# Kernel tuning notes

Measured on AMD Instinct MI355X. Metric: run time of the kernel, lower is better.

Reference implementation:

```python
import jax, jax.numpy as jnp
import numpy as np

N = 50000        # num_nodes
E = 200000       # num_edges
NODE_IN = 16
EDGE_IN = 8
H = 128          # hidden_dim (also per-head channels in GATConv)
HEADS = 4
L = 3            # num_layers
EPS = 1e-5
NEG_SLOPE = 0.2  # PyG GATConv default


def layer_norm(x, g, b):
    mu = jnp.mean(x, axis=-1, keepdims=True)
    v = jnp.var(x, axis=-1, keepdims=True)
    return (x - mu) * jax.lax.rsqrt(v + EPS) * g + b


def batch_norm_eval(x, g, b, rm, rv):
    return (x - rm) * jax.lax.rsqrt(rv + EPS) * g + b


def gat_layer(x, src, dst, W, a_src, a_dst, bias):
    # x: [N, H] -> per-head features [N, HEADS, H]
    xh = (x @ W).reshape(N, HEADS, H)
    al_src = jnp.sum(xh * a_src, axis=-1)  # [N, HEADS]
    al_dst = jnp.sum(xh * a_dst, axis=-1)  # [N, HEADS]
    alpha = jax.nn.leaky_relu(al_src[src] + al_dst[dst], NEG_SLOPE)  # [E', HEADS]
    # segment softmax over edges grouped by destination node
    m = jax.ops.segment_max(alpha, dst, num_segments=N)
    e = jnp.exp(alpha - m[dst])
    s = jax.ops.segment_sum(e, dst, num_segments=N)
    a = e / (s[dst] + 1e-16)
    msg = xh[src] * a[:, :, None]                 # [E', HEADS, H]
    out = jax.ops.segment_sum(msg, dst, num_segments=N)  # [N, HEADS, H]
    return jnp.mean(out, axis=1) + bias           # concat=False -> head mean


def setup_inputs() -> dict:
    key = jax.random.key(0)
    ks = jax.random.split(key, 24)
    s = 0.1
    inp = {
        "x": jax.random.normal(ks[0], (N, NODE_IN), jnp.float32),
        "edge_index": jax.random.randint(ks[1], (2, E), 0, N, jnp.int32),
        "edge_attr": jax.random.normal(ks[2], (E, EDGE_IN), jnp.float32),
        "shock_mask_nodes": jax.random.randint(ks[3], (N,), 0, 2, jnp.int32),
        # node encoder
        "enc_w": jax.random.normal(ks[4], (NODE_IN + 2, H), jnp.float32) * s,
        "enc_b": jnp.zeros((H,), jnp.float32),
        "enc_ln_g": jnp.ones((H,), jnp.float32),
        "enc_ln_b": jnp.zeros((H,), jnp.float32),
        # GAT layers (stacked over L)
        "gat_w": jax.random.normal(ks[5], (L, H, HEADS * H), jnp.float32) * s,
        "gat_att_src": jax.random.normal(ks[6], (L, HEADS, H), jnp.float32) * s,
        "gat_att_dst": jax.random.normal(ks[7], (L, HEADS, H), jnp.float32) * s,
        "gat_bias": jnp.zeros((L, H), jnp.float32),
        # BatchNorm (eval mode: running stats)
        "bn_g": jnp.ones((L, H), jnp.float32),
        "bn_b": jnp.zeros((L, H), jnp.float32),
        "bn_mean": jax.random.normal(ks[8], (L, H), jnp.float32) * 0.01,
        "bn_var": jnp.ones((L, H), jnp.float32),
        # edge MLP: (2H + EDGE_IN) -> H -> H//2 -> 1
        "em1_w": jax.random.normal(ks[9], (2 * H + EDGE_IN, H), jnp.float32) * s,
        "em1_b": jnp.zeros((H,), jnp.float32),
        "em_ln_g": jnp.ones((H,), jnp.float32),
        "em_ln_b": jnp.zeros((H,), jnp.float32),
        "em2_w": jax.random.normal(ks[10], (H, H // 2), jnp.float32) * s,
        "em2_b": jnp.zeros((H // 2,), jnp.float32),
        "em3_w": jax.random.normal(ks[11], (H // 2, 1), jnp.float32) * s,
        "em3_b": jnp.zeros((1,), jnp.float32),
    }
    return inp


def reference(x, edge_index, edge_attr, shock_mask_nodes,
              enc_w, enc_b, enc_ln_g, enc_ln_b,
              gat_w, gat_att_src, gat_att_dst, gat_bias,
              bn_g, bn_b, bn_mean, bn_var,
              em1_w, em1_b, em_ln_g, em_ln_b,
              em2_w, em2_b, em3_w, em3_b):
    src, dst = edge_index[0], edge_index[1]
    shock = shock_mask_nodes.astype(jnp.float32)[:, None]  # [N,1]
    # downstream indicator: scatter_add shock[src] into tgt, binarize
    down = jax.ops.segment_sum(shock[src, 0], dst, num_segments=N)
    down = (down > 0).astype(jnp.float32)[:, None]
    xa = jnp.concatenate([x, shock, down], axis=1)  # [N, NODE_IN+2]
    # node encoder (dropout off in eval)
    h = jax.nn.relu(layer_norm(xa @ enc_w + enc_b, enc_ln_g, enc_ln_b))
    # add self loops once (PyG GATConv default add_self_loops=True)
    loop = jnp.arange(N, dtype=src.dtype)
    src_sl = jnp.concatenate([src, loop])
    dst_sl = jnp.concatenate([dst, loop])
    for i in range(L):
        h = gat_layer(h, src_sl, dst_sl, gat_w[i], gat_att_src[i], gat_att_dst[i], gat_bias[i])
        h = batch_norm_eval(h, bn_g[i], bn_b[i], bn_mean[i], bn_var[i])
        if i < L - 1:
            h = jax.nn.relu(h)
    # edge predictor (note: source uses raw edge_attr, not augmented)
    edge_input = jnp.concatenate([h[src], h[dst], edge_attr], axis=1)  # [E, 2H+EDGE_IN]
    z = jax.nn.relu(layer_norm(edge_input @ em1_w + em1_b, em_ln_g, em_ln_b))
    z = jax.nn.relu(z @ em2_w + em2_b)
    delta = (z @ em3_w + em3_b)[:, 0]  # [E]
    return delta
```

## Files before the change

kernel.cpp:

```cpp
#include <hip/hip_runtime.h>
#include <hip/hip_bf16.h>


#define N_NODES 50000
#define N_EDGES 200000
#define ETOT    (N_EDGES + N_NODES)
#define HID     128
#define LN_EPS  1e-5f
#define NEG     0.2f
#define NSB     196

typedef __hip_bfloat16 bf16;
typedef __attribute__((ext_vector_type(8))) short v8s;
typedef __attribute__((ext_vector_type(4))) float v4f;
#define MFMA(a, b, c) __builtin_amdgcn_mfma_f32_16x16x32_bf16(a, b, c, 0, 0, 0)

__device__ __forceinline__ float b2f(unsigned short s) {
    return __uint_as_float(((unsigned int)s) << 16);
}
__device__ __forceinline__ unsigned short f2b(float f) {
    __hip_bfloat16 h = __float2bfloat16(f);
    return *reinterpret_cast<unsigned short*>(&h);
}
__device__ __forceinline__ unsigned int pack2(float a, float b) {
    return (unsigned int)f2b(a) | ((unsigned int)f2b(b) << 16);
}
__device__ __forceinline__ float pread(const void* p, size_t i, int isbf) {
    if (isbf) return b2f(((const unsigned short*)p)[i]);
    return ((const float*)p)[i];
}

__global__ void k_fill(float* out, int n, float v) {
    int i = blockIdx.x * blockDim.x + threadIdx.x;
    if (i < n) out[i] = v;
}

__global__ void k_detect(const unsigned short* __restrict__ xbuf,
                         int* __restrict__ flag) {
    int sane = 0;
    for (int j = threadIdx.x; j < 4096; j += 64) {
        unsigned short v = xbuf[2 * j];
        int e = (v >> 7) & 0xFF;
        if (v == 0 || (e > 96 && e < 160)) sane++;
    }
    for (int off = 32; off > 0; off >>= 1) sane += __shfl_down(sane, off);
    if (threadIdx.x == 0) flag[0] = (sane * 10 >= 4096 * 9) ? 1 : 0;
}

struct PrepArgs {
    const void *encw, *encb, *enlg, *enlb, *gatw, *asrc, *adst, *bias,
               *bng, *bnb, *bnm, *bnv, *em1w, *em1b, *emlg, *emlb,
               *em2w, *em2b, *em3w, *em3b;
};
#define PREP_ITEMS (150000 + 8193 + 1024 + 196608 + 32768 + 8192 + 3072)
__global__ void k_prep(PrepArgs a, float* __restrict__ pool,
                       unsigned short* __restrict__ gwt,
                       unsigned short* __restrict__ uvt,
                       unsigned short* __restrict__ w2t,
                       float* __restrict__ wl,
                       float* __restrict__ down, int* __restrict__ deg,
                       int* __restrict__ fill, const int* __restrict__ flag) {
    int i = blockIdx.x * 256 + threadIdx.x;
    int bf = flag[0];
    if (i < 150000) {
        int which = i / 50000, idx = i - which * 50000;
        if (which == 0) down[idx] = 0.f;
        else if (which == 1) deg[idx] = 0;
        else fill[idx] = 0;
        return;
    }
    i -= 150000;
    if (i < 8193) {
        const void* s; int off;
        if      (i < 2304) { s = a.encw; off = 0;    }
        else if (i < 2432) { s = a.encb; off = 2304; }
        else if (i < 2560) { s = a.enlg; off = 2432; }
        else if (i < 2688) { s = a.enlb; off = 2560; }
        else if (i < 4224) { s = a.asrc; off = 2688; }
        else if (i < 5760) { s = a.adst; off = 4224; }
        else if (i < 6144) { s = a.bias; off = 5760; }
        else if (i < 6528) { s = a.bng;  off = 6144; }
        else if (i < 6912) { s = a.bnb;  off = 6528; }
        else if (i < 7296) { s = a.bnm;  off = 6912; }
        else if (i < 7680) { s = a.bnv;  off = 7296; }
        else if (i < 7808) { s = a.em1b; off = 7680; }
        else if (i < 7936) { s = a.emlg; off = 7808; }
        else if (i < 8064) { s = a.emlb; off = 7936; }
        else if (i < 8128) { s = a.em2b; off = 8064; }
        else if (i < 8192) { s = a.em3w; off = 8128; }
        else               { s = a.em3b; off = 8192; }
        pool[i] = pread(s, i - off, bf);
        return;
    }
    i -= 8193;
    if (i < 1024) {
        int k = i >> 7, c = i & 127;
        pool[8200 + i] = pread(a.em1w, (size_t)(256 + k) * 128 + c, bf);
        return;
    }
    i -= 1024;
    if (i < 196608) {
        int L = i >> 16, rem = i & 65535, c = rem >> 9, k = rem & 511;
        gwt[i] = f2b(pread(a.gatw,
            (size_t)L * 65536 + (size_t)(k & 127) * 512 + (k >> 7) * 128 + c, bf));
        return;
    }
    i -= 196608;
    if (i < 32768) {
        int n = i >> 7, k = i & 127;
        float v = (n < 128) ? pread(a.em1w, (size_t)k * 128 + n, bf)
                            : pread(a.em1w, (size_t)(128 + k) * 128 + (n - 128), bf);
        uvt[i] = f2b(v);
        return;
    }
    i -= 32768;
    if (i < 8192) {
        int n = i >> 7, k = i & 127;
        w2t[i] = f2b(pread(a.em2w, (size_t)k * 64 + n, bf));
        return;
    }
    i -= 8192;
    if (i < 3072) {
        int L = i >> 10, rem = i & 1023, sd = rem >> 9, hh = (rem >> 7) & 3,
            kk = rem & 127;
        const void* av = sd ? a.adst : a.asrc;
        float acc = 0.f;
        for (int c = 0; c < 128; c++)
            acc += pread(a.gatw,
                       (size_t)L * 65536 + (size_t)kk * 512 + hh * 128 + c, bf)
                 * pread(av, (size_t)L * 512 + hh * 128 + c, bf);
        wl[i] = acc;
    }
}

__global__ void k_graph(const int* __restrict__ ei, const int* __restrict__ shock,
                        float* __restrict__ down, int* __restrict__ deg) {
    int e = blockIdx.x * blockDim.x + threadIdx.x;
    if (e < ETOT) {
        int d = (e < N_EDGES) ? ei[N_EDGES + e] : (e - N_EDGES);
        atomicAdd(&deg[d], 1);
        if (e < N_EDGES && shock[ei[e]] != 0) down[d] = 1.f;
    }
}

__global__ __launch_bounds__(256) void k_scan1(
        const int* __restrict__ deg, int* __restrict__ bsum) {
    __shared__ int red[4];
    int b = blockIdx.x, t = threadIdx.x, lane = t & 63, w = t >> 6;
    int idx = b * 256 + t;
    int v = (idx < N_NODES) ? deg[idx] : 0;
#pragma unroll
    for (int off = 1; off < 64; off <<= 1) v += __shfl_xor(v, off);
    if (lane == 0) red[w] = v;
    __syncthreads();
    if (t == 0) bsum[b] = red[0] + red[1] + red[2] + red[3];
}

__global__ __launch_bounds__(256) void k_scan2(
        const int* __restrict__ deg, const int* __restrict__ bsum,
        int* __restrict__ row_start) {
    __shared__ int red[4];
    __shared__ int wsum[4];
    int b = blockIdx.x, t = threadIdx.x, lane = t & 63, w = t >> 6;
    int pv = (t < b) ? bsum[t] : 0;
    int sm = pv;
#pragma unroll
    for (int off = 1; off < 64; off <<= 1) sm += __shfl_xor(sm, off);
    if (lane == 0) red[w] = sm;
    int idx = b * 256 + t;
    int v = (idx < N_NODES) ? deg[idx] : 0;
    int inc = v;
#pragma unroll
    for (int off = 1; off < 64; off <<= 1) {
        int u = __shfl_up(inc, off);
        if (lane >= off) inc += u;
    }
    if (lane == 63) wsum[w] = inc;
    __syncthreads();
    int boff = red[0] + red[1] + red[2] + red[3];
    int wo = 0;
#pragma unroll
    for (int i = 0; i < 4; i++) if (i < w) wo += wsum[i];
    if (idx < N_NODES) row_start[idx] = boff + wo + (inc - v);
    if (b == 0 && t == 0) row_start[N_NODES] = ETOT;
}

__global__ void k_csr(const int* __restrict__ ei, const int* __restrict__ row_start,
                      int* __restrict__ fill, int* __restrict__ csr_src) {
    int e = blockIdx.x * blockDim.x + threadIdx.x;
    if (e < ETOT) {
        int s, d;
        if (e < N_EDGES) { s = ei[e]; d = ei[N_EDGES + e]; }
        else             { s = e - N_EDGES; d = s; }
        int pos = row_start[d] + atomicAdd(&fill[d], 1);
        csr_src[pos] = s;
    }
}

__global__ __launch_bounds__(256) void k_encoder(
        const void* __restrict__ xraw, const int* __restrict__ flag,
        const int* __restrict__ shock, const float* __restrict__ down,
        const float* __restrict__ enc_w, const float* __restrict__ enc_b,
        const float* __restrict__ ln_g, const float* __restrict__ ln_b,
        unsigned short* __restrict__ h) {
    __shared__ float sw[2304];
    __shared__ float sp[384];
    int t = threadIdx.x;
    for (int i = t; i < 2304; i += 256) sw[i] = enc_w[i];
    if (t < 128)      sp[t] = enc_b[t];
    else if (t < 256) sp[t] = ln_g[t - 128];
    if (t < 128)      sp[256 + t] = ln_b[t];
    __syncthreads();

    int w = t >> 6, l = t & 63;
    int n = blockIdx.x * 4 + w;
    int bf = flag[0];
    int c0 = 2 * l, c1 = c0 + 1;

    float xv = (l < 16) ? pread(xraw, (size_t)n * 16 + l, bf) : 0.f;
    float xs = (float)shock[n];
    float xd = down[n];

    float a0 = sp[c0], a1 = sp[c1];
#pragma unroll
    for (int k = 0; k < 16; k++) {
        float xk = __shfl(xv, k);
        a0 = fmaf(xk, sw[k * HID + c0], a0);
        a1 = fmaf(xk, sw[k * HID + c1], a1);
    }
    a0 = fmaf(xs, sw[16 * HID + c0], a0); a1 = fmaf(xs, sw[16 * HID + c1], a1);
    a0 = fmaf(xd, sw[17 * HID + c0], a0); a1 = fmaf(xd, sw[17 * HID + c1], a1);

    float s = a0 + a1, q = a0 * a0 + a1 * a1;
#pragma unroll
    for (int off = 1; off < 64; off <<= 1) {
        s += __shfl_xor(s, off);
        q += __shfl_xor(q, off);
    }
    float mu = s * (1.f / 128.f);
    float var = q * (1.f / 128.f) - mu * mu;
    float rstd = rsqrtf(var + LN_EPS);
    float v0 = fmaxf((a0 - mu) * rstd * sp[128 + c0] + sp[256 + c0], 0.f);
    float v1 = fmaxf((a1 - mu) * rstd * sp[128 + c1] + sp[256 + c1], 0.f);
    *(unsigned int*)&h[(size_t)n * HID + c0] = pack2(v0, v1);
}

__global__ __launch_bounds__(256) void k_logits(
        const unsigned short* __restrict__ h, const float* __restrict__ wl,
        float* __restrict__ al_s, float* __restrict__ al_d) {
    __shared__ float wls[1024];
    int t = threadIdx.x;
    for (int i = t; i < 1024; i += 256) wls[i] = wl[i];
    __syncthreads();
    int lane = t & 63, w = t >> 6, l15 = lane & 15, q = lane >> 4;
    int n = blockIdx.x * 16 + w * 4 + q;
    v8s hv = *(const v8s*)&h[(size_t)n * 128 + l15 * 8];
    float hf[8];
#pragma unroll
    for (int m = 0; m < 8; m++) hf[m] = b2f((unsigned short)hv[m]);
    float p[8] = {};
#pragma unroll
    for (int j = 0; j < 8; j++) {
        float4 wa = *(const float4*)&wls[j * 128 + l15 * 8];
        float4 wb = *(const float4*)&wls[j * 128 + l15 * 8 + 4];
        p[j] = fmaf(hf[0], wa.x, p[j]); p[j] = fmaf(hf[1], wa.y, p[j]);
        p[j] = fmaf(hf[2], wa.z, p[j]); p[j] = fmaf(hf[3], wa.w, p[j]);
        p[j] = fmaf(hf[4], wb.x, p[j]); p[j] = fmaf(hf[5], wb.y, p[j]);
        p[j] = fmaf(hf[6], wb.z, p[j]); p[j] = fmaf(hf[7], wb.w, p[j]);
    }
#pragma unroll
    for (int off = 1; off < 16; off <<= 1)
#pragma unroll
        for (int j = 0; j < 8; j++) p[j] += __shfl_xor(p[j], off);
    if (l15 == 0) {
        float4 vs = {p[0], p[1], p[2], p[3]};
        float4 vd = {p[4], p[5], p[6], p[7]};
        *(float4*)&al_s[n * 4] = vs;
        *(float4*)&al_d[n * 4] = vd;
    }
}

__global__ __launch_bounds__(256) void k_agg2(
        const unsigned short* __restrict__ h, const float* __restrict__ al_src,
        const float* __restrict__ al_dst,
        const int* __restrict__ row_start, const int* __restrict__ csr_src,
        unsigned short* __restrict__ agg) {
    int w = threadIdx.x >> 6, l = threadIdx.x & 63;
    int n = blockIdx.x * 4 + w;
    int r0 = row_start[n], r1 = row_start[n + 1];
    float4 ad4 = *(const float4*)&al_dst[n * 4];
    float s0 = 0.f, s1 = 0.f, s2 = 0.f, s3 = 0.f;
    float acc[4][2] = {};
    int last = r1 - 1;
    int i0 = csr_src[r0];
    int i1 = csr_src[(r0 + 1 < r1) ? r0 + 1 : last];
    float4 aC = *(const float4*)&al_src[i0 * 4];
    unsigned int hC = *(const unsigned int*)&h[(size_t)i0 * 128 + 2 * l];
    for (int j = r0; j < r1; j++) {
        int i2 = csr_src[(j + 2 < r1) ? j + 2 : last];
        float4 aN = *(const float4*)&al_src[i1 * 4];
        unsigned int hN = *(const unsigned int*)&h[(size_t)i1 * 128 + 2 * l];
        float h0 = b2f((unsigned short)(hC & 0xFFFFu));
        float h1 = b2f((unsigned short)(hC >> 16));
        float t0 = aC.x + ad4.x; t0 = (t0 >= 0.f) ? t0 : NEG * t0;
        float t1 = aC.y + ad4.y; t1 = (t1 >= 0.f) ? t1 : NEG * t1;
        float t2 = aC.z + ad4.z; t2 = (t2 >= 0.f) ? t2 : NEG * t2;
        float t3 = aC.w + ad4.w; t3 = (t3 >= 0.f) ? t3 : NEG * t3;
        float e0 = __expf(t0), e1 = __expf(t1), e2 = __expf(t2), e3 = __expf(t3);
        s0 += e0; s1 += e1; s2 += e2; s3 += e3;
        acc[0][0] = fmaf(e0, h0, acc[0][0]); acc[0][1] = fmaf(e0, h1, acc[0][1]);
        acc[1][0] = fmaf(e1, h0, acc[1][0]); acc[1][1] = fmaf(e1, h1, acc[1][1]);
        acc[2][0] = fmaf(e2, h0, acc[2][0]); acc[2][1] = fmaf(e2, h1, acc[2][1]);
        acc[3][0] = fmaf(e3, h0, acc[3][0]); acc[3][1] = fmaf(e3, h1, acc[3][1]);
        aC = aN; hC = hN; i1 = i2;
    }
    float inv0 = 1.f / (s0 + 1e-16f), inv1 = 1.f / (s1 + 1e-16f);
    float inv2 = 1.f / (s2 + 1e-16f), inv3 = 1.f / (s3 + 1e-16f);
    size_t base = (size_t)n * 512 + 2 * l;
    *(unsigned int*)&agg[base]       = pack2(acc[0][0] * inv0, acc[0][1] * inv0);
    *(unsigned int*)&agg[base + 128] = pack2(acc[1][0] * inv1, acc[1][1] * inv1);
    *(unsigned int*)&agg[base + 256] = pack2(acc[2][0] * inv2, acc[2][1] * inv2);
    *(unsigned int*)&agg[base + 384] = pack2(acc[3][0] * inv3, acc[3][1] * inv3);
}

__global__ __launch_bounds__(256, 4) void k_gemm2(
        const unsigned short* __restrict__ A,
        const unsigned short* __restrict__ Wt,
        const float* __restrict__ bias,
        const float* __restrict__ bn_g, const float* __restrict__ bn_b,
        const float* __restrict__ bn_m, const float* __restrict__ bn_v,
        unsigned short* __restrict__ hout, int relu_flag) {
    __shared__ __align__(16) unsigned short As[64 * 136];
    int t = threadIdx.x;
    int lane = t & 63, w = t >> 6, l15 = lane & 15, q = lane >> 4;
    int m0 = blockIdx.x * 64;
    int c0 = w * 32 + 2 * l15, c1 = c0 + 1;

    v4f acc[4][2] = {};
#pragma unroll 1
    for (int kc = 0; kc < 4; kc++) {
        if (kc) __syncthreads();
#pragma unroll
        for (int it = 0; it < 4; it++) {
            int c = t + it * 256;
            int row = c >> 4, ch = c & 15;
            v8s val = {0, 0, 0, 0, 0, 0, 0, 0};
            if (m0 + row < N_NODES)
                val = *(const v8s*)&A[(size_t)(m0 + row) * 512 + kc * 128 + ch * 8];
            *(v8s*)&As[row * 136 + ch * 8] = val;
        }
        __syncthreads();
#pragma unroll
        for (int kt = 0; kt < 4; kt++) {
            v8s b0 = *(const v8s*)&Wt[(size_t)c0 * 512 + kc * 128 + kt * 32 + q * 8];
            v8s b1 = *(const v8s*)&Wt[(size_t)c1 * 512 + kc * 128 + kt * 32 + q * 8];
#pragma unroll
            for (int mt = 0; mt < 4; mt++) {
                v8s a = *(const v8s*)&As[(mt * 16 + l15) * 136 + kt * 32 + q * 8];
                acc[mt][0] = MFMA(a, b0, acc[mt][0]);
                acc[mt][1] = MFMA(a, b1, acc[mt][1]);
            }
        }
    }
    float bi0 = bias[c0], bi1 = bias[c1];
    float sc0 = rsqrtf(bn_v[c0] + LN_EPS) * bn_g[c0];
    float sc1 = rsqrtf(bn_v[c1] + LN_EPS) * bn_g[c1];
    float sh0 = bn_b[c0] - bn_m[c0] * sc0;
    float sh1 = bn_b[c1] - bn_m[c1] * sc1;
#pragma unroll
    for (int mt = 0; mt < 4; mt++)
#pragma unroll
        for (int r = 0; r < 4; r++) {
            int node = m0 + mt * 16 + q * 4 + r;
            if (node < N_NODES) {
                float v0 = (0.25f * acc[mt][0][r] + bi0) * sc0 + sh0;
                float v1 = (0.25f * acc[mt][1][r] + bi1) * sc1 + sh1;
                if (relu_flag) { v0 = fmaxf(v0, 0.f); v1 = fmaxf(v1, 0.f); }
                *(unsigned int*)&hout[(size_t)node * 128 + c0] = pack2(v0, v1);
            }
        }
}

__global__ __launch_bounds__(256, 4) void k_uvgemm(
        const unsigned short* __restrict__ A, const unsigned short* __restrict__ Wt,
        unsigned short* __restrict__ UV) {
    __shared__ __align__(16) unsigned short As[64 * 136];
    int t = threadIdx.x;
    int lane = t & 63, w = t >> 6, l15 = lane & 15, q = lane >> 4;
    int m0 = blockIdx.x * 64, n0 = blockIdx.y * 128;
    int c0 = n0 + w * 32 + 2 * l15;

    v8s b[2][4];
#pragma unroll
    for (int nt = 0; nt < 2; nt++)
#pragma unroll
        for (int kt = 0; kt < 4; kt++)
            b[nt][kt] = *(const v8s*)&Wt[(size_t)(c0 + nt) * 128 + kt * 32 + q * 8];
#pragma unroll
    for (int it = 0; it < 4; it++) {
        int c = t + it * 256;
        int row = c >> 4, ch = c & 15;
        v8s val = {0, 0, 0, 0, 0, 0, 0, 0};
        if (m0 + row < N_NODES)
            val = *(const v8s*)&A[(size_t)(m0 + row) * 128 + ch * 8];
        *(v8s*)&As[row * 136 + ch * 8] = val;
    }
    __syncthreads();

    v4f acc[4][2] = {};
#pragma unroll
    for (int kt = 0; kt < 4; kt++)
#pragma unroll
        for (int mt = 0; mt < 4; mt++) {
            v8s a = *(const v8s*)&As[(mt * 16 + l15) * 136 + kt * 32 + q * 8];
            acc[mt][0] = MFMA(a, b[0][kt], acc[mt][0]);
            acc[mt][1] = MFMA(a, b[1][kt], acc[mt][1]);
        }
#pragma unroll
    for (int mt = 0; mt < 4; mt++)
#pragma unroll
        for (int r = 0; r < 4; r++) {
            int node = m0 + mt * 16 + q * 4 + r;
            if (node < N_NODES)
                *(unsigned int*)&UV[(size_t)node * 256 + c0] =
                    pack2(acc[mt][0][r], acc[mt][1][r]);
        }
}

__global__ __launch_bounds__(256) void k_edgemlp3(
        const unsigned short* __restrict__ UV, const int* __restrict__ ei,
        const void* __restrict__ eraw, const int* __restrict__ flag,
        const float* __restrict__ w1e, const float* __restrict__ em1b,
        const float* __restrict__ lng, const float* __restrict__ lnb,
        const unsigned short* __restrict__ w2t, const float* __restrict__ em2b,
        const float* __restrict__ em3w, const float* __restrict__ em3b,
        float* __restrict__ out) {
    __shared__ __align__(16) unsigned short za[64 * 136];
    __shared__ __align__(16) float w1e_s[1024];
    __shared__ __align__(16) unsigned short ea_s[64 * 8];
    __shared__ int idx_s[128];
    __shared__ float part[4][64];

    int t = threadIdx.x;
    int lane = t & 63, w = t >> 6, l15 = lane & 15, q = lane >> 4;
    int e0 = blockIdx.x * 64;
    int bf = flag[0];
    int cb = l15 * 8;

    float bc[8], lg[8], lb[8];
#pragma unroll
    for (int j = 0; j < 8; j++) {
        bc[j] = em1b[cb + j];
        lg[j] = lng[cb + j];
        lb[j] = lnb[cb + j];
    }

    for (int i = t; i < 1024; i += 256) w1e_s[i] = w1e[i];
    if (t < 64) {
        idx_s[t * 2]     = ei[e0 + t];
        idx_s[t * 2 + 1] = ei[N_EDGES + e0 + t];
        if (bf) {
            *(v8s*)&ea_s[t * 8] =
                *(const v8s*)((const unsigned short*)eraw + (size_t)(e0 + t) * 8);
        } else {
            short tmp[8];
#pragma unroll
            for (int j = 0; j < 8; j++)
                tmp[j] = (short)f2b(((const float*)eraw)[(size_t)(e0 + t) * 8 + j]);
            *(v8s*)&ea_s[t * 8] = *(const v8s*)tmp;
        }
    }
    __syncthreads();

    int elC = w * 16 + q;
    {
        int srcC = idx_s[elC * 2], dstC = idx_s[elC * 2 + 1];
        v8s uuC = *(const v8s*)&UV[(size_t)srcC * 256 + cb];
        v8s vvC = *(const v8s*)&UV[(size_t)dstC * 256 + 128 + cb];
        v8s eaC = *(const v8s*)&ea_s[elC * 8];
#pragma unroll 1
        for (int i = 0; i < 4; i++) {
            v8s uuN = uuC, vvN = vvC, eaN = eaC;
            if (i < 3) {
                int elN = elC + 4;
                int srcN = idx_s[elN * 2], dstN = idx_s[elN * 2 + 1];
                uuN = *(const v8s*)&UV[(size_t)srcN * 256 + cb];
                vvN = *(const v8s*)&UV[(size_t)dstN * 256 + 128 + cb];
                eaN = *(const v8s*)&ea_s[elN * 8];
            }
            float eaf[8];
#pragma unroll
            for (int k = 0; k < 8; k++) eaf[k] = b2f((unsigned short)eaC[k]);
            float e[8] = {};
#pragma unroll
            for (int k = 0; k < 8; k++) {
                float4 wa = *(const float4*)&w1e_s[k * 128 + cb];
                float4 wb = *(const float4*)&w1e_s[k * 128 + cb + 4];
                e[0] = fmaf(eaf[k], wa.x, e[0]);
                e[1] = fmaf(eaf[k], wa.y, e[1]);
                e[2] = fmaf(eaf[k], wa.z, e[2]);
                e[3] = fmaf(eaf[k], wa.w, e[3]);
                e[4] = fmaf(eaf[k], wb.x, e[4]);
                e[5] = fmaf(eaf[k], wb.y, e[5]);
                e[6] = fmaf(eaf[k], wb.z, e[6]);
                e[7] = fmaf(eaf[k], wb.w, e[7]);
            }
            float z[8];
            float s = 0.f, qq = 0.f;
#pragma unroll
            for (int j = 0; j < 8; j++) {
                float zz = b2f((unsigned short)uuC[j]) + b2f((unsigned short)vvC[j])
                         + e[j] + bc[j];
                z[j] = zz;
                s += zz;
                qq = fmaf(zz, zz, qq);
            }
#pragma unroll
            for (int off = 1; off < 16; off <<= 1) {
                s  += __shfl_xor(s, off);
                qq += __shfl_xor(qq, off);
            }
            float mu = s * (1.f / 128.f);
            float var = qq * (1.f / 128.f) - mu * mu;
            float rstd = rsqrtf(var + LN_EPS);
            short o[8];
#pragma unroll
            for (int j = 0; j < 8; j++)
                o[j] = (short)f2b(fmaxf((z[j] - mu) * rstd * lg[j] + lb[j], 0.f));
            *(v8s*)&za[elC * 136 + cb] = *(const v8s*)o;
            elC += 4; uuC = uuN; vvC = vvN; eaC = eaN;
        }
    }
    __syncthreads();

    v8s b2[4];
#pragma unroll
    for (int kt = 0; kt < 4; kt++)
        b2[kt] = *(const v8s*)&w2t[(size_t)(w * 16 + l15) * 128 + kt * 32 + q * 8];
    v4f acc2[4] = {};
#pragma unroll
    for (int kt = 0; kt < 4; kt++)
#pragma unroll
        for (int mt = 0; mt < 4; mt++) {
            v8s a = *(const v8s*)&za[(mt * 16 + l15) * 136 + kt * 32 + q * 8];
            acc2[mt] = MFMA(a, b2[kt], acc2[mt]);
        }

    {
        int col = w * 16 + l15;
        float b2c = em2b[col], w3c = em3w[col];
#pragma unroll
        for (int mt = 0; mt < 4; mt++)
#pragma unroll
            for (int r = 0; r < 4; r++) {
                float vv = fmaxf(acc2[mt][r] + b2c, 0.f) * w3c;
#pragma unroll
                for (int off = 1; off < 16; off <<= 1) vv += __shfl_xor(vv, off);
                if (l15 == 0) part[w][mt * 16 + q * 4 + r] = vv;
            }
    }
    __syncthreads();
    if (t < 64)
        out[e0 + t] = part[0][t] + part[1][t] + part[2][t] + part[3][t]
                    + em3b[0];
}

extern "C" __attribute__((visibility("default")))
void kernel_launch(void* const* d_in, const int* in_sizes, int n_in,
                   void* d_out, int out_size, void* d_ws, size_t ws_size,
                   hipStream_t stream) {
    float* out = (float*)d_out;

    static const int EXP_SIZES[24] = {
        800000, 400000, 1600000, 50000, 2304, 128, 128, 128,
        196608, 1536, 1536, 384, 384, 384, 384, 384,
        33792, 128, 128, 128, 8192, 64, 64, 1};
    bool ok = (n_in == 24) && (out_size == N_EDGES);
    if (ok) for (int i = 0; i < 24; i++) ok = ok && (in_sizes[i] == EXP_SIZES[i]);
    if (!ok) {
        k_fill<<<(out_size + 255) / 256, 256, 0, stream>>>(out, out_size, 4.0f);
        return;
    }
    if (ws_size < (size_t)68000000) {
        k_fill<<<(out_size + 255) / 256, 256, 0, stream>>>(out, out_size, 8.0f);
        return;
    }

    const int* ei    = (const int*)d_in[1];
    const int* shock = (const int*)d_in[3];

    char* ws = (char*)d_ws;
    unsigned short* h_bf  = (unsigned short*)(ws + 0);
    unsigned short* agg   = (unsigned short*)(ws + 12800000);
    unsigned short* UV    = agg;
    float* al_s    = (float*)(ws + 64000000);
    float* al_d    = (float*)(ws + 64800000);
    float* down    = (float*)(ws + 65600000);
    int*   deg     = (int*)  (ws + 65800000);
    int*   row_st  = (int*)  (ws + 66000000);
    int*   fill    = (int*)  (ws + 66200064);
    int*   csr_src = (int*)  (ws + 66400064);
    int*   flag    = (int*)  (ws + 67400064);
    unsigned short* gwt = (unsigned short*)(ws + 67400128);
    unsigned short* uvt = (unsigned short*)(ws + 67793344);
    unsigned short* w2t = (unsigned short*)(ws + 67858880);
    float* pool    = (float*)(ws + 67875264);
    int*   bsum    = (int*)  (ws + 67912160);
    float* wl      = (float*)(ws + 67912960);

    float* cencw = pool + 0;    float* cencb = pool + 2304;
    float* cenlg = pool + 2432; float* cenlb = pool + 2560;
    float* cbias = pool + 5760; float* cbng  = pool + 6144;
    float* cbnb  = pool + 6528; float* cbnm  = pool + 6912;
    float* cbnv  = pool + 7296; float* cem1b = pool + 7680;
    float* cemlg = pool + 7808; float* cemlb = pool + 7936;
    float* cem2b = pool + 8064; float* cem3w = pool + 8128;
    float* cem3b = pool + 8192;
    float* w1e   = pool + 8200;

    k_detect<<<1, 64, 0, stream>>>((const unsigned short*)d_in[0], flag);

    PrepArgs pa;
    pa.encw = d_in[4];  pa.encb = d_in[5];  pa.enlg = d_in[6];  pa.enlb = d_in[7];
    pa.gatw = d_in[8];  pa.asrc = d_in[9];  pa.adst = d_in[10]; pa.bias = d_in[11];
    pa.bng  = d_in[12]; pa.bnb  = d_in[13]; pa.bnm  = d_in[14]; pa.bnv  = d_in[15];
    pa.em1w = d_in[16]; pa.em1b = d_in[17]; pa.emlg = d_in[18]; pa.emlb = d_in[19];
    pa.em2w = d_in[20]; pa.em2b = d_in[21]; pa.em3w = d_in[22]; pa.em3b = d_in[23];
    k_prep<<<(PREP_ITEMS + 255) / 256, 256, 0, stream>>>(
        pa, pool, gwt, uvt, w2t, wl, down, deg, fill, flag);

    k_graph<<<(ETOT + 255) / 256, 256, 0, stream>>>(ei, shock, down, deg);
    k_scan1<<<NSB, 256, 0, stream>>>(deg, bsum);
    k_scan2<<<NSB, 256, 0, stream>>>(deg, bsum, row_st);
    k_csr<<<(ETOT + 255) / 256, 256, 0, stream>>>(ei, row_st, fill, csr_src);
    k_encoder<<<N_NODES / 4, 256, 0, stream>>>(
        d_in[0], flag, shock, down, cencw, cencb, cenlg, cenlb, h_bf);
    for (int i = 0; i < 3; i++) {
        k_logits<<<N_NODES / 16, 256, 0, stream>>>(
            h_bf, wl + (size_t)i * 1024, al_s, al_d);
        k_agg2<<<N_NODES / 4, 256, 0, stream>>>(
            h_bf, al_s, al_d, row_st, csr_src, agg);
        k_gemm2<<<782, 256, 0, stream>>>(
            agg, gwt + (size_t)i * 65536,
            cbias + i * 128, cbng + i * 128, cbnb + i * 128,
            cbnm + i * 128, cbnv + i * 128, h_bf, (i < 2) ? 1 : 0);
    }
    k_uvgemm<<<dim3(782, 2), 256, 0, stream>>>(h_bf, uvt, UV);
    k_edgemlp3<<<N_EDGES / 64, 256, 0, stream>>>(
        UV, ei, d_in[2], flag, w1e, cem1b, cemlg, cemlb,
        w2t, cem2b, cem3w, cem3b, out);
}
```

Measured before the change: 502.7 us.

## Fuse attention logits into encoder and GEMM epilogue, widen aggregation loads

```diff
diff --git a/kernel.cpp b/kernel.cpp
--- a/kernel.cpp
+++ b/kernel.cpp
@@ -52,12 +52,14 @@
                *bng, *bnb, *bnm, *bnv, *em1w, *em1b, *emlg, *emlb,
                *em2w, *em2b, *em3w, *em3b;
 };
-#define PREP_ITEMS (150000 + 8193 + 1024 + 196608 + 32768 + 8192 + 3072)
+#define PREP_ITEMS (150000 + 8193 + 1024 + 196608 + 32768 + 8192 + 3072 + 6144)
 __global__ void k_prep(PrepArgs a, float* __restrict__ pool,
                        unsigned short* __restrict__ gwt,
                        unsigned short* __restrict__ uvt,
                        unsigned short* __restrict__ w2t,
                        float* __restrict__ wl,
+                       unsigned short* __restrict__ wlhi,
+                       unsigned short* __restrict__ wllo,
                        float* __restrict__ down, int* __restrict__ deg,
                        int* __restrict__ fill, const int* __restrict__ flag) {
     int i = blockIdx.x * 256 + threadIdx.x;
@@ -130,6 +132,23 @@
                        (size_t)L * 65536 + (size_t)kk * 512 + hh * 128 + c, bf)
                  * pread(av, (size_t)L * 512 + hh * 128 + c, bf);
         wl[i] = acc;
+        return;
+    }
+    i -= 3072;
+    if (i < 6144) {
+        int L = i >> 11, rem = i & 2047, j = rem >> 7, kk = rem & 127;
+        float d = 0.f;
+        if (j < 8) {
+            int sd = j >> 2, hh = j & 3;
+            const void* av = sd ? a.adst : a.asrc;
+            for (int c = 0; c < 128; c++)
+                d += pread(a.gatw,
+                         (size_t)L * 65536 + (size_t)kk * 512 + hh * 128 + c, bf)
+                   * pread(av, (size_t)L * 512 + hh * 128 + c, bf);
+        }
+        unsigned short hi = f2b(d);
+        wlhi[i] = hi;
+        wllo[i] = f2b(d - b2f(hi));
     }
 }
 
@@ -202,11 +221,15 @@
         const int* __restrict__ shock, const float* __restrict__ down,
         const float* __restrict__ enc_w, const float* __restrict__ enc_b,
         const float* __restrict__ ln_g, const float* __restrict__ ln_b,
-        unsigned short* __restrict__ h) {
+        const float* __restrict__ wl0,
+        unsigned short* __restrict__ h,
+        float* __restrict__ al_s, float* __restrict__ al_d) {
     __shared__ float sw[2304];
     __shared__ float sp[384];
+    __shared__ float swl[1024];
     int t = threadIdx.x;
     for (int i = t; i < 2304; i += 256) sw[i] = enc_w[i];
+    for (int i = t; i < 1024; i += 256) swl[i] = wl0[i];
     if (t < 128)      sp[t] = enc_b[t];
     else if (t < 256) sp[t] = ln_g[t - 128];
     if (t < 128)      sp[256 + t] = ln_b[t];
@@ -242,37 +265,20 @@
     float rstd = rsqrtf(var + LN_EPS);
     float v0 = fmaxf((a0 - mu) * rstd * sp[128 + c0] + sp[256 + c0], 0.f);
     float v1 = fmaxf((a1 - mu) * rstd * sp[128 + c1] + sp[256 + c1], 0.f);
-    *(unsigned int*)&h[(size_t)n * HID + c0] = pack2(v0, v1);
-}
-
-__global__ __launch_bounds__(256) void k_logits(
-        const unsigned short* __restrict__ h, const float* __restrict__ wl,
-        float* __restrict__ al_s, float* __restrict__ al_d) {
-    __shared__ float wls[1024];
-    int t = threadIdx.x;
-    for (int i = t; i < 1024; i += 256) wls[i] = wl[i];
-    __syncthreads();
-    int lane = t & 63, w = t >> 6, l15 = lane & 15, q = lane >> 4;
-    int n = blockIdx.x * 16 + w * 4 + q;
-    v8s hv = *(const v8s*)&h[(size_t)n * 128 + l15 * 8];
-    float hf[8];
-#pragma unroll
-    for (int m = 0; m < 8; m++) hf[m] = b2f((unsigned short)hv[m]);
-    float p[8] = {};
-#pragma unroll
-    for (int j = 0; j < 8; j++) {
-        float4 wa = *(const float4*)&wls[j * 128 + l15 * 8];
-        float4 wb = *(const float4*)&wls[j * 128 + l15 * 8 + 4];
-        p[j] = fmaf(hf[0], wa.x, p[j]); p[j] = fmaf(hf[1], wa.y, p[j]);
-        p[j] = fmaf(hf[2], wa.z, p[j]); p[j] = fmaf(hf[3], wa.w, p[j]);
-        p[j] = fmaf(hf[4], wb.x, p[j]); p[j] = fmaf(hf[5], wb.y, p[j]);
-        p[j] = fmaf(hf[6], wb.z, p[j]); p[j] = fmaf(hf[7], wb.w, p[j]);
-    }
-#pragma unroll
-    for (int off = 1; off < 16; off <<= 1)
+    unsigned int pv = pack2(v0, v1);
+    *(unsigned int*)&h[(size_t)n * HID + c0] = pv;
+
+    float v0r = b2f((unsigned short)(pv & 0xFFFFu));
+    float v1r = b2f((unsigned short)(pv >> 16));
+    float p[8];
+#pragma unroll
+    for (int j = 0; j < 8; j++)
+        p[j] = v0r * swl[j * 128 + c0] + v1r * swl[j * 128 + c1];
+#pragma unroll
+    for (int off = 1; off < 64; off <<= 1)
 #pragma unroll
         for (int j = 0; j < 8; j++) p[j] += __shfl_xor(p[j], off);
-    if (l15 == 0) {
+    if (l == 0) {
         float4 vs = {p[0], p[1], p[2], p[3]};
         float4 vd = {p[4], p[5], p[6], p[7]};
         *(float4*)&al_s[n * 4] = vs;
@@ -280,47 +286,78 @@
     }
 }
 
-__global__ __launch_bounds__(256) void k_agg2(
+__global__ __launch_bounds__(256) void k_agg4(
         const unsigned short* __restrict__ h, const float* __restrict__ al_src,
         const float* __restrict__ al_dst,
         const int* __restrict__ row_start, const int* __restrict__ csr_src,
         unsigned short* __restrict__ agg) {
     int w = threadIdx.x >> 6, l = threadIdx.x & 63;
     int n = blockIdx.x * 4 + w;
+    int g = l >> 4, c = l & 15;
     int r0 = row_start[n], r1 = row_start[n + 1];
+    int last = r1 - 1;
+    int iters = (r1 - r0 + 3) >> 2;
     float4 ad4 = *(const float4*)&al_dst[n * 4];
     float s0 = 0.f, s1 = 0.f, s2 = 0.f, s3 = 0.f;
-    float acc[4][2] = {};
-    int last = r1 - 1;
-    int i0 = csr_src[r0];
-    int i1 = csr_src[(r0 + 1 < r1) ? r0 + 1 : last];
-    float4 aC = *(const float4*)&al_src[i0 * 4];
-    unsigned int hC = *(const unsigned int*)&h[(size_t)i0 * 128 + 2 * l];
-    for (int j = r0; j < r1; j++) {
-        int i2 = csr_src[(j + 2 < r1) ? j + 2 : last];
-        float4 aN = *(const float4*)&al_src[i1 * 4];
-        unsigned int hN = *(const unsigned int*)&h[(size_t)i1 * 128 + 2 * l];
-        float h0 = b2f((unsigned short)(hC & 0xFFFFu));
-        float h1 = b2f((unsigned short)(hC >> 16));
+    float acc[4][8] = {};
+
+    int j0 = r0 + g;
+    int vC = (j0 <= last) ? 1 : 0;
+    int jc = vC ? j0 : last;
+    int iC = csr_src[jc];
+    float4 aC = *(const float4*)&al_src[iC * 4];
+    v8s hC = *(const v8s*)&h[(size_t)iC * 128 + c * 8];
+
+#pragma unroll 1
+    for (int it = 0; it < iters; it++) {
+        float4 aN = aC; v8s hN = hC; int vN = 0;
+        if (it + 1 < iters) {
+            int jn = r0 + (it + 1) * 4 + g;
+            vN = (jn <= last) ? 1 : 0;
+            jn = vN ? jn : last;
+            int iN = csr_src[jn];
+            aN = *(const float4*)&al_src[iN * 4];
+            hN = *(const v8s*)&h[(size_t)iN * 128 + c * 8];
+        }
         float t0 = aC.x + ad4.x; t0 = (t0 >= 0.f) ? t0 : NEG * t0;
         float t1 = aC.y + ad4.y; t1 = (t1 >= 0.f) ? t1 : NEG * t1;
         float t2 = aC.z + ad4.z; t2 = (t2 >= 0.f) ? t2 : NEG * t2;
         float t3 = aC.w + ad4.w; t3 = (t3 >= 0.f) ? t3 : NEG * t3;
-        float e0 = __expf(t0), e1 = __expf(t1), e2 = __expf(t2), e3 = __expf(t3);
+        float m = (float)vC;
+        float e0 = __expf(t0) * m, e1 = __expf(t1) * m,
+              e2 = __expf(t2) * m, e3 = __expf(t3) * m;
         s0 += e0; s1 += e1; s2 += e2; s3 += e3;
-        acc[0][0] = fmaf(e0, h0, acc[0][0]); acc[0][1] = fmaf(e0, h1, acc[0][1]);
-        acc[1][0] = fmaf(e1, h0, acc[1][0]); acc[1][1] = fmaf(e1, h1, acc[1][1]);
-        acc[2][0] = fmaf(e2, h0, acc[2][0]); acc[2][1] = fmaf(e2, h1, acc[2][1]);
-        acc[3][0] = fmaf(e3, h0, acc[3][0]); acc[3][1] = fmaf(e3, h1, acc[3][1]);
-        aC = aN; hC = hN; i1 = i2;
-    }
-    float inv0 = 1.f / (s0 + 1e-16f), inv1 = 1.f / (s1 + 1e-16f);
-    float inv2 = 1.f / (s2 + 1e-16f), inv3 = 1.f / (s3 + 1e-16f);
-    size_t base = (size_t)n * 512 + 2 * l;
-    *(unsigned int*)&agg[base]       = pack2(acc[0][0] * inv0, acc[0][1] * inv0);
-    *(unsigned int*)&agg[base + 128] = pack2(acc[1][0] * inv1, acc[1][1] * inv1);
-    *(unsigned int*)&agg[base + 256] = pack2(acc[2][0] * inv2, acc[2][1] * inv2);
-    *(unsigned int*)&agg[base + 384] = pack2(acc[3][0] * inv3, acc[3][1] * inv3);
+#pragma unroll
+        for (int i = 0; i < 8; i++) {
+            float hv = b2f((unsigned short)hC[i]);
+            acc[0][i] = fmaf(e0, hv, acc[0][i]);
+            acc[1][i] = fmaf(e1, hv, acc[1][i]);
+            acc[2][i] = fmaf(e2, hv, acc[2][i]);
+            acc[3][i] = fmaf(e3, hv, acc[3][i]);
+        }
+        aC = aN; hC = hN; vC = vN;
+    }
+    s0 += __shfl_xor(s0, 16); s0 += __shfl_xor(s0, 32);
+    s1 += __shfl_xor(s1, 16); s1 += __shfl_xor(s1, 32);
+    s2 += __shfl_xor(s2, 16); s2 += __shfl_xor(s2, 32);
+    s3 += __shfl_xor(s3, 16); s3 += __shfl_xor(s3, 32);
+#pragma unroll
+    for (int hh = 0; hh < 4; hh++)
+#pragma unroll
+        for (int i = 0; i < 8; i++) {
+            acc[hh][i] += __shfl_xor(acc[hh][i], 16);
+            acc[hh][i] += __shfl_xor(acc[hh][i], 32);
+        }
+    float sg = (g == 0) ? s0 : (g == 1) ? s1 : (g == 2) ? s2 : s3;
+    float inv = 1.f / (sg + 1e-16f);
+    short o[8];
+#pragma unroll
+    for (int i = 0; i < 8; i++) {
+        float av = (g == 0) ? acc[0][i] : (g == 1) ? acc[1][i]
+                 : (g == 2) ? acc[2][i] : acc[3][i];
+        o[i] = (short)f2b(av * inv);
+    }
+    *(v8s*)&agg[(size_t)n * 512 + g * 128 + c * 8] = *(const v8s*)o;
 }
 
 __global__ __launch_bounds__(256, 4) void k_gemm2(
@@ -329,39 +366,68 @@
         const float* __restrict__ bias,
         const float* __restrict__ bn_g, const float* __restrict__ bn_b,
         const float* __restrict__ bn_m, const float* __restrict__ bn_v,
-        unsigned short* __restrict__ hout, int relu_flag) {
-    __shared__ __align__(16) unsigned short As[64 * 136];
+        unsigned short* __restrict__ hout, int relu_flag,
+        const unsigned short* __restrict__ wlhi,
+        const unsigned short* __restrict__ wllo,
+        float* __restrict__ al_s, float* __restrict__ al_d, int logit_flag) {
+    __shared__ __align__(16) unsigned short As[2][64 * 136];
     int t = threadIdx.x;
     int lane = t & 63, w = t >> 6, l15 = lane & 15, q = lane >> 4;
     int m0 = blockIdx.x * 64;
     int c0 = w * 32 + 2 * l15, c1 = c0 + 1;
 
+    v8s st[4];
+#pragma unroll
+    for (int it = 0; it < 4; it++) {
+        int cc = t + it * 256, row = cc >> 4, ch = cc & 15;
+        v8s val = {0, 0, 0, 0, 0, 0, 0, 0};
+        if (m0 + row < N_NODES)
+            val = *(const v8s*)&A[(size_t)(m0 + row) * 512 + ch * 8];
+        st[it] = val;
+    }
+#pragma unroll
+    for (int it = 0; it < 4; it++) {
+        int cc = t + it * 256, row = cc >> 4, ch = cc & 15;
+        *(v8s*)&As[0][row * 136 + ch * 8] = st[it];
+    }
+    __syncthreads();
+
     v4f acc[4][2] = {};
-#pragma unroll 1
+#pragma unroll
     for (int kc = 0; kc < 4; kc++) {
-        if (kc) __syncthreads();
-#pragma unroll
-        for (int it = 0; it < 4; it++) {
-            int c = t + it * 256;
-            int row = c >> 4, ch = c & 15;
-            v8s val = {0, 0, 0, 0, 0, 0, 0, 0};
-            if (m0 + row < N_NODES)
-                val = *(const v8s*)&A[(size_t)(m0 + row) * 512 + kc * 128 + ch * 8];
-            *(v8s*)&As[row * 136 + ch * 8] = val;
-        }
-        __syncthreads();
+        if (kc < 3) {
+#pragma unroll
+            for (int it = 0; it < 4; it++) {
+                int cc = t + it * 256, row = cc >> 4, ch = cc & 15;
+                v8s val = {0, 0, 0, 0, 0, 0, 0, 0};
+                if (m0 + row < N_NODES)
+                    val = *(const v8s*)&A[(size_t)(m0 + row) * 512
+                                          + (kc + 1) * 128 + ch * 8];
+                st[it] = val;
+            }
+        }
 #pragma unroll
         for (int kt = 0; kt < 4; kt++) {
             v8s b0 = *(const v8s*)&Wt[(size_t)c0 * 512 + kc * 128 + kt * 32 + q * 8];
             v8s b1 = *(const v8s*)&Wt[(size_t)c1 * 512 + kc * 128 + kt * 32 + q * 8];
 #pragma unroll
             for (int mt = 0; mt < 4; mt++) {
-                v8s a = *(const v8s*)&As[(mt * 16 + l15) * 136 + kt * 32 + q * 8];
+                v8s a = *(const v8s*)&As[kc & 1][(mt * 16 + l15) * 136
+                                                 + kt * 32 + q * 8];
                 acc[mt][0] = MFMA(a, b0, acc[mt][0]);
                 acc[mt][1] = MFMA(a, b1, acc[mt][1]);
             }
         }
-    }
+        if (kc < 3) {
+#pragma unroll
+            for (int it = 0; it < 4; it++) {
+                int cc = t + it * 256, row = cc >> 4, ch = cc & 15;
+                *(v8s*)&As[(kc + 1) & 1][row * 136 + ch * 8] = st[it];
+            }
+        }
+        __syncthreads();
+    }
+
     float bi0 = bias[c0], bi1 = bias[c1];
     float sc0 = rsqrtf(bn_v[c0] + LN_EPS) * bn_g[c0];
     float sc1 = rsqrtf(bn_v[c1] + LN_EPS) * bn_g[c1];
@@ -371,14 +437,40 @@
     for (int mt = 0; mt < 4; mt++)
 #pragma unroll
         for (int r = 0; r < 4; r++) {
-            int node = m0 + mt * 16 + q * 4 + r;
-            if (node < N_NODES) {
-                float v0 = (0.25f * acc[mt][0][r] + bi0) * sc0 + sh0;
-                float v1 = (0.25f * acc[mt][1][r] + bi1) * sc1 + sh1;
-                if (relu_flag) { v0 = fmaxf(v0, 0.f); v1 = fmaxf(v1, 0.f); }
-                *(unsigned int*)&hout[(size_t)node * 128 + c0] = pack2(v0, v1);
+            int row = mt * 16 + q * 4 + r;
+            int node = m0 + row;
+            float v0 = (0.25f * acc[mt][0][r] + bi0) * sc0 + sh0;
+            float v1 = (0.25f * acc[mt][1][r] + bi1) * sc1 + sh1;
+            if (relu_flag) { v0 = fmaxf(v0, 0.f); v1 = fmaxf(v1, 0.f); }
+            unsigned int pv = pack2(v0, v1);
+            if (node < N_NODES)
+                *(unsigned int*)&hout[(size_t)node * 128 + c0] = pv;
+            if (logit_flag)
+                *(unsigned int*)&As[0][row * 136 + c0] = pv;
+        }
+
+    if (logit_flag) {
+        __syncthreads();
+        v4f accL = {0.f, 0.f, 0.f, 0.f};
+#pragma unroll
+        for (int kt = 0; kt < 4; kt++) {
+            v8s a  = *(const v8s*)&As[0][(w * 16 + l15) * 136 + kt * 32 + q * 8];
+            v8s bh = *(const v8s*)&wlhi[(size_t)l15 * 128 + kt * 32 + q * 8];
+            v8s bl = *(const v8s*)&wllo[(size_t)l15 * 128 + kt * 32 + q * 8];
+            accL = MFMA(a, bh, accL);
+            accL = MFMA(a, bl, accL);
+        }
+        if (l15 < 8) {
+#pragma unroll
+            for (int r = 0; r < 4; r++) {
+                int node = m0 + w * 16 + q * 4 + r;
+                if (node < N_NODES) {
+                    if (l15 < 4) al_s[node * 4 + l15] = accL[r];
+                    else         al_d[node * 4 + (l15 - 4)] = accL[r];
+                }
             }
         }
+    }
 }
 
 __global__ __launch_bounds__(256, 4) void k_uvgemm(
@@ -472,64 +564,53 @@
     }
     __syncthreads();
 
-    int elC = w * 16 + q;
-    {
-        int srcC = idx_s[elC * 2], dstC = idx_s[elC * 2 + 1];
-        v8s uuC = *(const v8s*)&UV[(size_t)srcC * 256 + cb];
-        v8s vvC = *(const v8s*)&UV[(size_t)dstC * 256 + 128 + cb];
-        v8s eaC = *(const v8s*)&ea_s[elC * 8];
 #pragma unroll 1
-        for (int i = 0; i < 4; i++) {
-            v8s uuN = uuC, vvN = vvC, eaN = eaC;
-            if (i < 3) {
-                int elN = elC + 4;
-                int srcN = idx_s[elN * 2], dstN = idx_s[elN * 2 + 1];
-                uuN = *(const v8s*)&UV[(size_t)srcN * 256 + cb];
-                vvN = *(const v8s*)&UV[(size_t)dstN * 256 + 128 + cb];
-                eaN = *(const v8s*)&ea_s[elN * 8];
-            }
-            float eaf[8];
-#pragma unroll
-            for (int k = 0; k < 8; k++) eaf[k] = b2f((unsigned short)eaC[k]);
-            float e[8] = {};
-#pragma unroll
-            for (int k = 0; k < 8; k++) {
-                float4 wa = *(const float4*)&w1e_s[k * 128 + cb];
-                float4 wb = *(const float4*)&w1e_s[k * 128 + cb + 4];
-                e[0] = fmaf(eaf[k], wa.x, e[0]);
-                e[1] = fmaf(eaf[k], wa.y, e[1]);
-                e[2] = fmaf(eaf[k], wa.z, e[2]);
-                e[3] = fmaf(eaf[k], wa.w, e[3]);
-                e[4] = fmaf(eaf[k], wb.x, e[4]);
-                e[5] = fmaf(eaf[k], wb.y, e[5]);
-                e[6] = fmaf(eaf[k], wb.z, e[6]);
-                e[7] = fmaf(eaf[k], wb.w, e[7]);
-            }
-            float z[8];
-            float s = 0.f, qq = 0.f;
-#pragma unroll
-            for (int j = 0; j < 8; j++) {
-                float zz = b2f((unsigned short)uuC[j]) + b2f((unsigned short)vvC[j])
-                         + e[j] + bc[j];
-                z[j] = zz;
-                s += zz;
-                qq = fmaf(zz, zz, qq);
-            }
-#pragma unroll
-            for (int off = 1; off < 16; off <<= 1) {
-                s  += __shfl_xor(s, off);
-                qq += __shfl_xor(qq, off);
-            }
-            float mu = s * (1.f / 128.f);
-            float var = qq * (1.f / 128.f) - mu * mu;
-            float rstd = rsqrtf(var + LN_EPS);
-            short o[8];
-#pragma unroll
-            for (int j = 0; j < 8; j++)
-                o[j] = (short)f2b(fmaxf((z[j] - mu) * rstd * lg[j] + lb[j], 0.f));
-            *(v8s*)&za[elC * 136 + cb] = *(const v8s*)o;
-            elC += 4; uuC = uuN; vvC = vvN; eaC = eaN;
-        }
+    for (int i = 0; i < 4; i++) {
+        int el = w * 16 + i * 4 + q;
+        int src = idx_s[el * 2], dst = idx_s[el * 2 + 1];
+        v8s uu = *(const v8s*)&UV[(size_t)src * 256 + cb];
+        v8s vv = *(const v8s*)&UV[(size_t)dst * 256 + 128 + cb];
+        v8s ea8 = *(const v8s*)&ea_s[el * 8];
+        float eaf[8];
+#pragma unroll
+        for (int k = 0; k < 8; k++) eaf[k] = b2f((unsigned short)ea8[k]);
+        float e[8] = {};
+#pragma unroll
+        for (int k = 0; k < 8; k++) {
+            float4 wa = *(const float4*)&w1e_s[k * 128 + cb];
+            float4 wb = *(const float4*)&w1e_s[k * 128 + cb + 4];
+            e[0] = fmaf(eaf[k], wa.x, e[0]);
+            e[1] = fmaf(eaf[k], wa.y, e[1]);
+            e[2] = fmaf(eaf[k], wa.z, e[2]);
+            e[3] = fmaf(eaf[k], wa.w, e[3]);
+            e[4] = fmaf(eaf[k], wb.x, e[4]);
+            e[5] = fmaf(eaf[k], wb.y, e[5]);
+            e[6] = fmaf(eaf[k], wb.z, e[6]);
+            e[7] = fmaf(eaf[k], wb.w, e[7]);
+        }
+        float z[8];
+        float s = 0.f, qq = 0.f;
+#pragma unroll
+        for (int j = 0; j < 8; j++) {
+            float zz = b2f((unsigned short)uu[j]) + b2f((unsigned short)vv[j])
+                     + e[j] + bc[j];
+            z[j] = zz;
+            s += zz;
+            qq = fmaf(zz, zz, qq);
+        }
+#pragma unroll
+        for (int off = 1; off < 16; off <<= 1) {
+            s  += __shfl_xor(s, off);
+            qq += __shfl_xor(qq, off);
+        }
+        float mu = s * (1.f / 128.f);
+        float var = qq * (1.f / 128.f) - mu * mu;
+        float rstd = rsqrtf(var + LN_EPS);
+        short o[8];
+#pragma unroll
+        for (int j = 0; j < 8; j++)
+            o[j] = (short)f2b(fmaxf((z[j] - mu) * rstd * lg[j] + lb[j], 0.f));
+        *(v8s*)&za[el * 136 + cb] = *(const v8s*)o;
     }
     __syncthreads();
 
@@ -607,6 +688,8 @@
     float* pool    = (float*)(ws + 67875264);
     int*   bsum    = (int*)  (ws + 67912160);
     float* wl      = (float*)(ws + 67912960);
+    unsigned short* wlhi = (unsigned short*)(ws + 67925248);
+    unsigned short* wllo = (unsigned short*)(ws + 67937536);
 
     float* cencw = pool + 0;    float* cencb = pool + 2304;
     float* cenlg = pool + 2432; float* cenlb = pool + 2560;
@@ -627,23 +710,24 @@
     pa.em1w = d_in[16]; pa.em1b = d_in[17]; pa.emlg = d_in[18]; pa.emlb = d_in[19];
     pa.em2w = d_in[20]; pa.em2b = d_in[21]; pa.em3w = d_in[22]; pa.em3b = d_in[23];
     k_prep<<<(PREP_ITEMS + 255) / 256, 256, 0, stream>>>(
-        pa, pool, gwt, uvt, w2t, wl, down, deg, fill, flag);
+        pa, pool, gwt, uvt, w2t, wl, wlhi, wllo, down, deg, fill, flag);
 
     k_graph<<<(ETOT + 255) / 256, 256, 0, stream>>>(ei, shock, down, deg);
     k_scan1<<<NSB, 256, 0, stream>>>(deg, bsum);
     k_scan2<<<NSB, 256, 0, stream>>>(deg, bsum, row_st);
     k_csr<<<(ETOT + 255) / 256, 256, 0, stream>>>(ei, row_st, fill, csr_src);
     k_encoder<<<N_NODES / 4, 256, 0, stream>>>(
-        d_in[0], flag, shock, down, cencw, cencb, cenlg, cenlb, h_bf);
+        d_in[0], flag, shock, down, cencw, cencb, cenlg, cenlb, wl,
+        h_bf, al_s, al_d);
     for (int i = 0; i < 3; i++) {
-        k_logits<<<N_NODES / 16, 256, 0, stream>>>(
-            h_bf, wl + (size_t)i * 1024, al_s, al_d);
-        k_agg2<<<N_NODES / 4, 256, 0, stream>>>(
+        k_agg4<<<N_NODES / 4, 256, 0, stream>>>(
             h_bf, al_s, al_d, row_st, csr_src, agg);
         k_gemm2<<<782, 256, 0, stream>>>(
             agg, gwt + (size_t)i * 65536,
             cbias + i * 128, cbng + i * 128, cbnb + i * 128,
-            cbnm + i * 128, cbnv + i * 128, h_bf, (i < 2) ? 1 : 0);
+            cbnm + i * 128, cbnv + i * 128, h_bf, (i < 2) ? 1 : 0,
+            wlhi + (size_t)(i + 1) * 2048, wllo + (size_t)(i + 1) * 2048,
+            al_s, al_d, (i < 2) ? 1 : 0);
     }
     k_uvgemm<<<dim3(782, 2), 256, 0, stream>>>(h_bf, uvt, UV);
     k_edgemlp3<<<N_EDGES / 64, 256, 0, stream>>>(
```

New measurement: 490.1 us. 1.03x faster.
